# Kernel optimization log

Measured on AMD Instinct MI355X. Metric: run time of the kernel, lower is better.

The kernel has to match this reference:

```python
import jax, jax.numpy as jnp
import numpy as np

N = 100_000   # total nodes per graph batch
E = 400_000   # directed edges per graph batch
G = 1024      # number of graphs
F_IN = 90


def _lin_init(key, fan_in, fan_out):
    s = 1.0 / np.sqrt(fan_in)
    kW, kb = jax.random.split(key)
    W = jax.random.uniform(kW, (fan_in, fan_out), jnp.float32, -s, s)
    b = jax.random.uniform(kb, (fan_out,), jnp.float32, -s, s)
    return W, b


def setup_inputs() -> dict:
    key = jax.random.key(0)
    ks = jax.random.split(key, 16)
    batch = (jnp.arange(N, dtype=jnp.int32) * G // N).astype(jnp.int32)
    inp = {
        'x1': jax.random.normal(ks[0], (N, F_IN), jnp.float32),
        'edge_index1': jax.random.randint(ks[1], (2, E), 0, N, jnp.int32),
        'batch1': batch,
        'x2': jax.random.normal(ks[2], (N, F_IN), jnp.float32),
        'edge_index2': jax.random.randint(ks[3], (2, E), 0, N, jnp.int32),
        'batch2': batch,
    }
    W1, b1 = _lin_init(ks[4], 90, 128)
    W2, b2 = _lin_init(ks[5], 128, 256)
    W3, b3 = _lin_init(ks[6], 256, 256)
    W4, b4 = _lin_init(ks[7], 256, 256)
    fc1_W, fc1_b = _lin_init(ks[8], 1024, 512)
    fc2_W, fc2_b = _lin_init(ks[9], 512, 256)
    fc3_W, fc3_b = _lin_init(ks[10], 256, 1)
    inp.update(W1=W1, b1=b1, W2=W2, b2=b2, W3=W3, b3=b3, W4=W4, b4=b4,
               fc1_W=fc1_W, fc1_b=fc1_b, fc2_W=fc2_W, fc2_b=fc2_b,
               fc3_W=fc3_W, fc3_b=fc3_b)
    return inp


def _gcn(x, W, b, src, dst, dinv):
    # GCNConv: D^{-1/2} (A + I) D^{-1/2} X W + b  (self-loops added)
    h = x @ W                                   # [N, F_out]
    norm = dinv[src] * dinv[dst]                # [E]
    agg = jax.ops.segment_sum(h[src] * norm[:, None], dst, num_segments=N)
    agg = agg + h * (dinv * dinv)[:, None]      # self-loop term
    return agg + b


def _drug_encoder(x, edge_index, batch, W1, b1, W2, b2, W3, b3, W4, b4):
    src, dst = edge_index[0], edge_index[1]
    # degree with self-loops (PyG gcn_norm)
    deg = jax.ops.segment_sum(jnp.ones(src.shape[0], x.dtype), dst, num_segments=N) + 1.0
    dinv = jax.lax.rsqrt(deg)
    x = jax.nn.relu(_gcn(x, W1, b1, src, dst, dinv))
    x = jax.nn.relu(_gcn(x, W2, b2, src, dst, dinv))
    x = jax.nn.relu(_gcn(x, W3, b3, src, dst, dinv))
    x = jax.nn.relu(_gcn(x, W4, b4, src, dst, dinv))
    gmax = jax.ops.segment_max(x, batch, num_segments=G)
    cnt = jax.ops.segment_sum(jnp.ones(N, x.dtype), batch, num_segments=G)
    gmean = jax.ops.segment_sum(x, batch, num_segments=G) / cnt[:, None]
    return jnp.concatenate([gmax, gmean], axis=1)   # [G, 512]


def reference(x1, edge_index1, batch1, x2, edge_index2, batch2,
              W1, b1, W2, b2, W3, b3, W4, b4,
              fc1_W, fc1_b, fc2_W, fc2_b, fc3_W, fc3_b):
    h1 = _drug_encoder(x1, edge_index1, batch1, W1, b1, W2, b2, W3, b3, W4, b4)
    h2 = _drug_encoder(x2, edge_index2, batch2, W1, b1, W2, b2, W3, b3, W4, b4)
    x = jnp.concatenate([h1 - h2, h2 - h1], axis=1)   # [G, 1024]
    x = jax.nn.relu(x @ fc1_W + fc1_b)                # dropout = identity (eval)
    x = jax.nn.relu(x @ fc2_W + fc2_b)
    x = jnp.tanh(x @ fc3_W + fc3_b)
    return x                                          # [G, 1]
```

## Files before the change

kernel.cpp:

```cpp
#include <hip/hip_runtime.h>
#include <hip/hip_bf16.h>

#define NN 100000
#define EE 400000
#define GG 1024

typedef _Float16 half_t;
typedef _Float16 f16x8 __attribute__((ext_vector_type(8)));
typedef float f32x4 __attribute__((ext_vector_type(4)));

#define GLOAD_LDS(g, l) \
    __builtin_amdgcn_global_load_lds((const __attribute__((address_space(1))) void*)(g), \
                                     (__attribute__((address_space(3))) void*)(l), 16, 0, 0)


__global__ void k_count(const int* __restrict__ ei, int* __restrict__ deg) {
    int e = blockIdx.x * blockDim.x + threadIdx.x;
    if (e < EE) atomicAdd(&deg[ei[EE + e]], 1);
}

__global__ void k_scan_bsum(const int* __restrict__ deg, int* __restrict__ bsum) {
    __shared__ int lds[256];
    int t = threadIdx.x;
    int base = blockIdx.x * 1024 + t * 4;
    int s = 0;
#pragma unroll
    for (int i = 0; i < 4; ++i) { int idx = base + i; s += (idx < NN) ? deg[idx] : 0; }
    lds[t] = s;
    __syncthreads();
    for (int off = 128; off > 0; off >>= 1) {
        if (t < off) lds[t] += lds[t + off];
        __syncthreads();
    }
    if (t == 0) bsum[blockIdx.x] = lds[0];
}

__global__ void k_scan_write(const int* __restrict__ deg, const int* __restrict__ bsum,
                             int* __restrict__ rowptr) {
    __shared__ int lds[256];
    __shared__ int blockoff;
    int t = threadIdx.x;
    if (t == 0) {
        int off = 0;
        for (int b = 0; b < (int)blockIdx.x; ++b) off += bsum[b];
        blockoff = off;
    }
    int base = blockIdx.x * 1024 + t * 4;
    int v[4]; int ts = 0;
#pragma unroll
    for (int i = 0; i < 4; ++i) { int idx = base + i; v[i] = (idx < NN) ? deg[idx] : 0; ts += v[i]; }
    lds[t] = ts;
    __syncthreads();
    for (int off = 1; off < 256; off <<= 1) {
        int x = (t >= off) ? lds[t - off] : 0;
        __syncthreads();
        lds[t] += x;
        __syncthreads();
    }
    int excl = lds[t] - ts + blockoff;
#pragma unroll
    for (int i = 0; i < 4; ++i) {
        int idx = base + i;
        if (idx < NN) rowptr[idx] = excl;
        excl += v[i];
    }
    if (blockIdx.x == 0 && t == 0) rowptr[NN] = EE;
}

__global__ void k_dinv(const int* __restrict__ deg, float* __restrict__ dinv) {
    int i = blockIdx.x * blockDim.x + threadIdx.x;
    if (i < NN) dinv[i] = rsqrtf((float)deg[i] + 1.0f);
}

__global__ void k_fill(const int* __restrict__ ei, const int* __restrict__ rowptr,
                       int* __restrict__ cnt, int* __restrict__ col) {
    int e = blockIdx.x * blockDim.x + threadIdx.x;
    if (e < EE) {
        int s = ei[e], d = ei[EE + e];
        int pos = rowptr[d] + atomicAdd(&cnt[d], 1);
        col[pos] = s;
    }
}


template <int F, int R, int KPAD>
__global__ void k_agg_split(const float* __restrict__ x, const float* __restrict__ dinv,
                            const int* __restrict__ rowptr, const int* __restrict__ col,
                            half_t* __restrict__ out) {
    int wave = threadIdx.x >> 6;
    int lane = threadIdx.x & 63;
    int n = blockIdx.x * 4 + wave;
    if (n >= NN) return;
    float dn = dinv[n];
    const float* xr = x + (size_t)n * F;
    float acc[R];
#pragma unroll
    for (int r = 0; r < R; ++r) {
        int f = lane + 64 * r;
        acc[r] = (f < F) ? dn * xr[f] : 0.f;
    }
    int j0 = rowptr[n], j1 = rowptr[n + 1];
    for (int j = j0; j < j1; ++j) {
        int s = col[j];
        float ds = dinv[s];
        const float* xs = x + (size_t)s * F;
#pragma unroll
        for (int r = 0; r < R; ++r) {
            int f = lane + 64 * r;
            if (f < F) acc[r] += ds * xs[f];
        }
    }
    half_t* o = out + (size_t)n * (2 * KPAD);
#pragma unroll
    for (int r = 0; r < R; ++r) {
        int f = lane + 64 * r;
        if (f < F) {
            float v = dn * acc[r];
            half_t h = (half_t)v;
            half_t l = (half_t)(v - (float)h);
            o[f] = h;
            o[KPAD + f] = l;
        } else if (f < KPAD) {
            o[f] = (half_t)0.f;
            o[KPAD + f] = (half_t)0.f;
        }
    }
}


template <int VW>
__global__ void k_agg_splitv(const float* __restrict__ x, const float* __restrict__ dinv,
                             const int* __restrict__ rowptr, const int* __restrict__ col,
                             half_t* __restrict__ out) {
    constexpr int F = 64 * VW;
    typedef float fvec __attribute__((ext_vector_type(VW)));
    int wave = threadIdx.x >> 6;
    int lane = threadIdx.x & 63;
    int n = blockIdx.x * 4 + wave;
    if (n >= NN) return;
    float dn = dinv[n];
    fvec acc = dn * ((const fvec*)(x + (size_t)n * F))[lane];
    int j0 = rowptr[n], j1 = rowptr[n + 1];
    for (int j = j0; j < j1; ++j) {
        int s = col[j];
        float ds = dinv[s];
        acc += ds * ((const fvec*)(x + (size_t)s * F))[lane];
    }
    half_t* o = out + (size_t)n * (2 * F);
    half_t hv[VW], lv[VW];
#pragma unroll
    for (int i = 0; i < VW; ++i) {
        float v = dn * acc[i];
        hv[i] = (half_t)v;
        lv[i] = (half_t)(v - (float)hv[i]);
    }
#pragma unroll
    for (int i = 0; i < VW; ++i) o[lane * VW + i] = hv[i];
#pragma unroll
    for (int i = 0; i < VW; ++i) o[F + lane * VW + i] = lv[i];
}


__global__ void k_wprep(const float* __restrict__ W, half_t* __restrict__ Bt,
                        int K, int Kpad, int Nc) {
    int t = blockIdx.x * 256 + threadIdx.x;
    if (t >= Nc * Kpad) return;
    int n = t / Kpad, kp = t % Kpad;
    half_t h = (half_t)0.f, l = (half_t)0.f;
    if (kp < K) {
        float w = W[(size_t)kp * Nc + n];
        h = (half_t)w;
        l = (half_t)(w - (float)h);
    }
    half_t* o = Bt + (size_t)n * 3 * Kpad;
    o[kp] = h;
    o[Kpad + kp] = h;
    o[2 * Kpad + kp] = l;
}


__global__ void k_split(const float* __restrict__ in, half_t* __restrict__ out, int K) {
    int t = blockIdx.x * 256 + threadIdx.x;
    int row = t / K, k = t % K;
    float v = in[t];
    half_t h = (half_t)v;
    half_t l = (half_t)(v - (float)h);
    half_t* o = out + (size_t)row * 2 * K;
    o[k] = h;
    o[K + k] = l;
}


template <bool RELU>
__global__ __launch_bounds__(256, 2)
void k_mgemm(const half_t* __restrict__ Ap, const half_t* __restrict__ Bt,
             const float* __restrict__ bias, float* __restrict__ C,
             int M, int Kpad, int Nc) {
    __shared__ half_t As[128 * 64];
    __shared__ half_t Bs[128 * 64];
    const int tid = threadIdx.x;
    const int wave = tid >> 6, lane = tid & 63;
    const int wm = wave >> 1, wn = wave & 1;
    const int bm = blockIdx.x * 128, bn = blockIdx.y * 128;
    const int KA = 2 * Kpad, KB = 3 * Kpad;
    const int nkt = KB >> 6;
    const int aTiles = KA >> 6;

    f32x4 acc[4][4] = {};

    const int srow = tid >> 3;
    const int ch = tid & 7;

    for (int kt = 0; kt < nkt; ++kt) {
        int ka0 = ((kt < aTiles) ? kt : (kt - aTiles)) << 6;
        int kb0 = kt << 6;
        __syncthreads();
#pragma unroll
        for (int i = 0; i < 4; ++i) {
            int rl = i * 32 + srow;
            int sch = ch ^ (rl & 7);
            int gr = bm + rl; if (gr >= M) gr = M - 1;
            const half_t* ga = Ap + (size_t)gr * KA + ka0 + sch * 8;
            GLOAD_LDS(ga, (char*)As + i * 4096 + wave * 1024);
        }
#pragma unroll
        for (int i = 0; i < 4; ++i) {
            int rl = i * 32 + srow;
            int sch = ch ^ (rl & 7);
            const half_t* gb = Bt + (size_t)(bn + rl) * KB + kb0 + sch * 8;
            GLOAD_LDS(gb, (char*)Bs + i * 4096 + wave * 1024);
        }
        __syncthreads();
#pragma unroll
        for (int s = 0; s < 2; ++s) {
            f16x8 af[4], bf[4];
#pragma unroll
            for (int i = 0; i < 4; ++i) {
                int row = wm * 64 + i * 16 + (lane & 15);
                int c = s * 4 + (lane >> 4);
                af[i] = *(const f16x8*)&As[row * 64 + ((c ^ (row & 7)) << 3)];
            }
#pragma unroll
            for (int j = 0; j < 4; ++j) {
                int row = wn * 64 + j * 16 + (lane & 15);
                int c = s * 4 + (lane >> 4);
                bf[j] = *(const f16x8*)&Bs[row * 64 + ((c ^ (row & 7)) << 3)];
            }
#pragma unroll
            for (int i = 0; i < 4; ++i)
#pragma unroll
                for (int j = 0; j < 4; ++j)
                    acc[i][j] = __builtin_amdgcn_mfma_f32_16x16x32_f16(af[i], bf[j], acc[i][j], 0, 0, 0);
        }
    }

#pragma unroll
    for (int i = 0; i < 4; ++i) {
#pragma unroll
        for (int j = 0; j < 4; ++j) {
            int cc = bn + wn * 64 + j * 16 + (lane & 15);
            float bv = bias[cc];
            int r0 = bm + wm * 64 + i * 16 + (lane >> 4) * 4;
#pragma unroll
            for (int q = 0; q < 4; ++q) {
                int gr = r0 + q;
                if (gr < M) {
                    float v = acc[i][j][q] + bv;
                    if (RELU) v = fmaxf(v, 0.f);
                    C[(size_t)gr * Nc + cc] = v;
                }
            }
        }
    }
}


__global__ void k_starts(const int* __restrict__ batch, int* __restrict__ gstart) {
    int i = blockIdx.x * blockDim.x + threadIdx.x;
    if (i >= NN) return;
    int b = batch[i];
    if (i == 0) {
        for (int g = 0; g <= b; ++g) gstart[g] = 0;
    } else {
        int pb = batch[i - 1];
        for (int g = pb + 1; g <= b; ++g) gstart[g] = i;
    }
    if (i == NN - 1) {
        for (int g = b + 1; g <= GG; ++g) gstart[g] = NN;
    }
}

__global__ void k_pool(const float* __restrict__ act, const int* __restrict__ gstart,
                       float* __restrict__ h) {
    int g = blockIdx.x;
    int f = threadIdx.x;
    int s = gstart[g], e = gstart[g + 1];
    float mx = 0.f, sm = 0.f;
    for (int i = s; i < e; ++i) {
        float v = act[(size_t)i * 256 + f];
        mx = fmaxf(mx, v);
        sm += v;
    }
    float cnt = (float)(e - s);
    h[(size_t)g * 512 + f] = mx;
    h[(size_t)g * 512 + 256 + f] = (cnt > 0.f) ? sm / cnt : 0.f;
}


__global__ void k_headin_split(const float* __restrict__ h, half_t* __restrict__ xh) {
    int t = blockIdx.x * blockDim.x + threadIdx.x;
    if (t >= GG * 1024) return;
    int g = t >> 10, j = t & 1023;
    const float* h1 = h + (size_t)g * 512;
    const float* h2 = h + (size_t)(GG + g) * 512;
    float v = (j < 512) ? (h1[j] - h2[j]) : (h2[j - 512] - h1[j - 512]);
    half_t hi = (half_t)v;
    half_t lo = (half_t)(v - (float)hi);
    half_t* o = xh + (size_t)g * 2048;
    o[j] = hi;
    o[1024 + j] = lo;
}

__global__ void k_fc3(const float* __restrict__ A, const float* __restrict__ W,
                      const float* __restrict__ b, float* __restrict__ out) {
    int g = blockIdx.x * 4 + (threadIdx.x >> 6);
    int lane = threadIdx.x & 63;
    const float* a = A + (size_t)g * 256;
    float p = a[lane] * W[lane] + a[lane + 64] * W[lane + 64]
            + a[lane + 128] * W[lane + 128] + a[lane + 192] * W[lane + 192];
    for (int off = 32; off > 0; off >>= 1) p += __shfl_down(p, off);
    if (lane == 0) out[g] = tanhf(p + b[0]);
}


extern "C" void kernel_launch(void* const* d_in, const int* in_sizes, int n_in,
                              void* d_out, int out_size, void* d_ws, size_t ws_size,
                              hipStream_t stream) {
    const float* x1  = (const float*)d_in[0];
    const int*   ei1 = (const int*)d_in[1];
    const int*   ba1 = (const int*)d_in[2];
    const float* x2  = (const float*)d_in[3];
    const int*   ei2 = (const int*)d_in[4];
    const int*   ba2 = (const int*)d_in[5];
    const float* W1 = (const float*)d_in[6];
    const float* b1 = (const float*)d_in[7];
    const float* W2 = (const float*)d_in[8];
    const float* b2 = (const float*)d_in[9];
    const float* W3 = (const float*)d_in[10];
    const float* b3 = (const float*)d_in[11];
    const float* W4 = (const float*)d_in[12];
    const float* b4 = (const float*)d_in[13];
    const float* fc1W = (const float*)d_in[14];
    const float* fc1b = (const float*)d_in[15];
    const float* fc2W = (const float*)d_in[16];
    const float* fc2b = (const float*)d_in[17];
    const float* fc3W = (const float*)d_in[18];
    const float* fc3b = (const float*)d_in[19];
    float* out = (float*)d_out;

    char* ws = (char*)d_ws;
    size_t off = 0;
    auto alloc = [&](size_t bytes) -> void* {
        void* p = (void*)(ws + off);
        off += (bytes + 255) & ~(size_t)255;
        return p;
    };
    int*    deg    = (int*)alloc(NN * sizeof(int));
    int*    rowptr = (int*)alloc((NN + 1) * sizeof(int));
    int*    cnt    = (int*)alloc(NN * sizeof(int));
    int*    col    = (int*)alloc(EE * sizeof(int));
    int*    bsum   = (int*)alloc(128 * sizeof(int));
    int*    gstart = (int*)alloc((GG + 1) * sizeof(int));
    float*  dinv   = (float*)alloc(NN * sizeof(float));
    half_t* Ap     = (half_t*)alloc((size_t)NN * 512 * sizeof(half_t));
    float*  act    = (float*)alloc((size_t)NN * 256 * sizeof(float));
    half_t* Bt1    = (half_t*)alloc((size_t)128 * 384 * sizeof(half_t));
    half_t* Bt2    = (half_t*)alloc((size_t)256 * 384 * sizeof(half_t));
    half_t* Bt3    = (half_t*)alloc((size_t)256 * 768 * sizeof(half_t));
    half_t* Bt4    = (half_t*)alloc((size_t)256 * 768 * sizeof(half_t));
    half_t* Btf1   = (half_t*)alloc((size_t)512 * 3072 * sizeof(half_t));
    half_t* Btf2   = (half_t*)alloc((size_t)256 * 1536 * sizeof(half_t));
    float*  hpool  = (float*)alloc((size_t)2 * GG * 512 * sizeof(float));
    half_t* xhs    = (half_t*)alloc((size_t)GG * 2048 * sizeof(half_t));
    float*  t1     = (float*)alloc((size_t)GG * 512 * sizeof(float));
    half_t* t1s    = (half_t*)alloc((size_t)GG * 1024 * sizeof(half_t));
    float*  t2     = (float*)alloc((size_t)GG * 256 * sizeof(float));

    int nsb = (NN + 1023) / 1024;
    int mt = (NN + 127) / 128;

    k_wprep<<<(128 * 128 + 255) / 256, 256, 0, stream>>>(W1, Bt1, 90, 128, 128);
    k_wprep<<<(256 * 128 + 255) / 256, 256, 0, stream>>>(W2, Bt2, 128, 128, 256);
    k_wprep<<<(256 * 256 + 255) / 256, 256, 0, stream>>>(W3, Bt3, 256, 256, 256);
    k_wprep<<<(256 * 256 + 255) / 256, 256, 0, stream>>>(W4, Bt4, 256, 256, 256);
    k_wprep<<<(512 * 1024 + 255) / 256, 256, 0, stream>>>(fc1W, Btf1, 1024, 1024, 512);
    k_wprep<<<(256 * 512 + 255) / 256, 256, 0, stream>>>(fc2W, Btf2, 512, 512, 256);

    for (int p = 0; p < 2; ++p) {
        const float* x   = p ? x2 : x1;
        const int*   ei  = p ? ei2 : ei1;
        const int*   bat = p ? ba2 : ba1;
        hipMemsetAsync(deg, 0, NN * sizeof(int), stream);
        hipMemsetAsync(cnt, 0, NN * sizeof(int), stream);
        k_count<<<(EE + 255) / 256, 256, 0, stream>>>(ei, deg);
        k_scan_bsum<<<nsb, 256, 0, stream>>>(deg, bsum);
        k_scan_write<<<nsb, 256, 0, stream>>>(deg, bsum, rowptr);
        k_dinv<<<(NN + 255) / 256, 256, 0, stream>>>(deg, dinv);
        k_fill<<<(EE + 255) / 256, 256, 0, stream>>>(ei, rowptr, cnt, col);
        k_starts<<<(NN + 255) / 256, 256, 0, stream>>>(bat, gstart);

        k_agg_split<90, 2, 128><<<(NN + 3) / 4, 256, 0, stream>>>(x, dinv, rowptr, col, Ap);
        k_mgemm<true><<<dim3(mt, 1), 256, 0, stream>>>(Ap, Bt1, b1, act, NN, 128, 128);
        k_agg_splitv<2><<<(NN + 3) / 4, 256, 0, stream>>>(act, dinv, rowptr, col, Ap);
        k_mgemm<true><<<dim3(mt, 2), 256, 0, stream>>>(Ap, Bt2, b2, act, NN, 128, 256);
        k_agg_splitv<4><<<(NN + 3) / 4, 256, 0, stream>>>(act, dinv, rowptr, col, Ap);
        k_mgemm<true><<<dim3(mt, 2), 256, 0, stream>>>(Ap, Bt3, b3, act, NN, 256, 256);
        k_agg_splitv<4><<<(NN + 3) / 4, 256, 0, stream>>>(act, dinv, rowptr, col, Ap);
        k_mgemm<true><<<dim3(mt, 2), 256, 0, stream>>>(Ap, Bt4, b4, act, NN, 256, 256);

        k_pool<<<GG, 256, 0, stream>>>(act, gstart, hpool + (size_t)p * GG * 512);
    }

    k_headin_split<<<(GG * 1024 + 255) / 256, 256, 0, stream>>>(hpool, xhs);
    k_mgemm<true><<<dim3(GG / 128, 4), 256, 0, stream>>>(xhs, Btf1, fc1b, t1, GG, 1024, 512);
    k_split<<<(GG * 512 + 255) / 256, 256, 0, stream>>>(t1, t1s, 512);
    k_mgemm<true><<<dim3(GG / 128, 2), 256, 0, stream>>>(t1s, Btf2, fc2b, t2, GG, 512, 256);
    k_fc3<<<GG / 4, 256, 0, stream>>>(t2, fc3W, fc3b, out);
}
```

Before: 1.463 ms.

## Batch CSR build for both graphs, fuse dinv into scan, unroll gather loops

Builds the CSR structure for both encoders in one pass: the degree count, scan, fill and graph-start kernels each run once over concatenated 2N/2E ranges, and dinv is computed inside the scan-write kernel. This removes several launches and memsets. The aggregation kernels unroll the neighbour loop by four so more independent gathers are in flight, and the layer-1 aggregation uses float2 loads over 45 lanes. Column indices for graph 2 stay local to that graph and are paired with an offset rowptr, which is consistent. The single-block serial prefix over bsum now covers twice as many blocks.

```diff
diff --git a/kernel.cpp b/kernel.cpp
--- a/kernel.cpp
+++ b/kernel.cpp
@@ -8,24 +8,30 @@
 typedef _Float16 half_t;
 typedef _Float16 f16x8 __attribute__((ext_vector_type(8)));
 typedef float f32x4 __attribute__((ext_vector_type(4)));
+typedef float f32x2 __attribute__((ext_vector_type(2)));
 
 #define GLOAD_LDS(g, l) \
     __builtin_amdgcn_global_load_lds((const __attribute__((address_space(1))) void*)(g), \
                                      (__attribute__((address_space(3))) void*)(l), 16, 0, 0)
 
 
-__global__ void k_count(const int* __restrict__ ei, int* __restrict__ deg) {
-    int e = blockIdx.x * blockDim.x + threadIdx.x;
-    if (e < EE) atomicAdd(&deg[ei[EE + e]], 1);
-}
-
-__global__ void k_scan_bsum(const int* __restrict__ deg, int* __restrict__ bsum) {
+__global__ void k_count2(const int* __restrict__ ei1, const int* __restrict__ ei2,
+                         int* __restrict__ deg) {
+    int e = blockIdx.x * 256 + threadIdx.x;
+    if (e >= 2 * EE) return;
+    int enc = e >= EE;
+    const int* ei = enc ? ei2 : ei1;
+    int le = e - enc * EE;
+    atomicAdd(&deg[enc * NN + ei[EE + le]], 1);
+}
+
+__global__ void k_scan_bsum(const int* __restrict__ deg, int* __restrict__ bsum, int total) {
     __shared__ int lds[256];
     int t = threadIdx.x;
     int base = blockIdx.x * 1024 + t * 4;
     int s = 0;
 #pragma unroll
-    for (int i = 0; i < 4; ++i) { int idx = base + i; s += (idx < NN) ? deg[idx] : 0; }
+    for (int i = 0; i < 4; ++i) { int idx = base + i; s += (idx < total) ? deg[idx] : 0; }
     lds[t] = s;
     __syncthreads();
     for (int off = 128; off > 0; off >>= 1) {
@@ -36,7 +42,8 @@
 }
 
 __global__ void k_scan_write(const int* __restrict__ deg, const int* __restrict__ bsum,
-                             int* __restrict__ rowptr) {
+                             int* __restrict__ rowptr, float* __restrict__ dinv,
+                             int total, int totedge) {
     __shared__ int lds[256];
     __shared__ int blockoff;
     int t = threadIdx.x;
@@ -48,7 +55,7 @@
     int base = blockIdx.x * 1024 + t * 4;
     int v[4]; int ts = 0;
 #pragma unroll
-    for (int i = 0; i < 4; ++i) { int idx = base + i; v[i] = (idx < NN) ? deg[idx] : 0; ts += v[i]; }
+    for (int i = 0; i < 4; ++i) { int idx = base + i; v[i] = (idx < total) ? deg[idx] : 0; ts += v[i]; }
     lds[t] = ts;
     __syncthreads();
     for (int off = 1; off < 256; off <<= 1) {
@@ -61,72 +68,92 @@
 #pragma unroll
     for (int i = 0; i < 4; ++i) {
         int idx = base + i;
-        if (idx < NN) rowptr[idx] = excl;
+        if (idx < total) {
+            rowptr[idx] = excl;
+            dinv[idx] = rsqrtf((float)v[i] + 1.0f);
+        }
         excl += v[i];
     }
-    if (blockIdx.x == 0 && t == 0) rowptr[NN] = EE;
-}
-
-__global__ void k_dinv(const int* __restrict__ deg, float* __restrict__ dinv) {
-    int i = blockIdx.x * blockDim.x + threadIdx.x;
-    if (i < NN) dinv[i] = rsqrtf((float)deg[i] + 1.0f);
-}
-
-__global__ void k_fill(const int* __restrict__ ei, const int* __restrict__ rowptr,
-                       int* __restrict__ cnt, int* __restrict__ col) {
-    int e = blockIdx.x * blockDim.x + threadIdx.x;
-    if (e < EE) {
-        int s = ei[e], d = ei[EE + e];
-        int pos = rowptr[d] + atomicAdd(&cnt[d], 1);
-        col[pos] = s;
-    }
-}
-
-
-template <int F, int R, int KPAD>
-__global__ void k_agg_split(const float* __restrict__ x, const float* __restrict__ dinv,
-                            const int* __restrict__ rowptr, const int* __restrict__ col,
-                            half_t* __restrict__ out) {
+    if (blockIdx.x == 0 && t == 0) rowptr[total] = totedge;
+}
+
+__global__ void k_fill2(const int* __restrict__ ei1, const int* __restrict__ ei2,
+                        const int* __restrict__ rowptr, int* __restrict__ cnt,
+                        int* __restrict__ colv) {
+    int e = blockIdx.x * 256 + threadIdx.x;
+    if (e >= 2 * EE) return;
+    int enc = e >= EE;
+    const int* ei = enc ? ei2 : ei1;
+    int le = e - enc * EE;
+    int s = ei[le], d = ei[EE + le];
+    int gd = enc * NN + d;
+    int pos = rowptr[gd] + atomicAdd(&cnt[gd], 1);
+    colv[pos] = s;
+}
+
+__global__ void k_starts2(const int* __restrict__ b1, const int* __restrict__ b2,
+                          int* __restrict__ gstart) {
+    int i = blockIdx.x * 256 + threadIdx.x;
+    if (i >= 2 * NN) return;
+    int enc = i >= NN;
+    int il = i - enc * NN;
+    const int* bat = enc ? b2 : b1;
+    int* gs = gstart + enc * (GG + 1);
+    int b = bat[il];
+    if (il == 0) {
+        for (int g = 0; g <= b; ++g) gs[g] = 0;
+    } else {
+        int pb = bat[il - 1];
+        for (int g = pb + 1; g <= b; ++g) gs[g] = il;
+    }
+    if (il == NN - 1) {
+        for (int g = b + 1; g <= GG; ++g) gs[g] = NN;
+    }
+}
+
+
+__global__ void k_agg90(const float* __restrict__ x, const float* __restrict__ dinv,
+                        const int* __restrict__ rowptr, const int* __restrict__ col,
+                        half_t* __restrict__ out) {
     int wave = threadIdx.x >> 6;
     int lane = threadIdx.x & 63;
     int n = blockIdx.x * 4 + wave;
     if (n >= NN) return;
+    bool al = lane < 45;
     float dn = dinv[n];
-    const float* xr = x + (size_t)n * F;
-    float acc[R];
-#pragma unroll
-    for (int r = 0; r < R; ++r) {
-        int f = lane + 64 * r;
-        acc[r] = (f < F) ? dn * xr[f] : 0.f;
-    }
+    f32x2 acc = {0.f, 0.f};
+    if (al) acc = dn * ((const f32x2*)(x + (size_t)n * 90))[lane];
     int j0 = rowptr[n], j1 = rowptr[n + 1];
-    for (int j = j0; j < j1; ++j) {
+    int j = j0;
+    for (; j + 4 <= j1; j += 4) {
+        int s0 = col[j], s1 = col[j + 1], s2 = col[j + 2], s3 = col[j + 3];
+        float d0 = dinv[s0], d1 = dinv[s1], d2 = dinv[s2], d3 = dinv[s3];
+        if (al) {
+            f32x2 v0 = ((const f32x2*)(x + (size_t)s0 * 90))[lane];
+            f32x2 v1 = ((const f32x2*)(x + (size_t)s1 * 90))[lane];
+            f32x2 v2 = ((const f32x2*)(x + (size_t)s2 * 90))[lane];
+            f32x2 v3 = ((const f32x2*)(x + (size_t)s3 * 90))[lane];
+            acc += d0 * v0;
+            acc += d1 * v1;
+            acc += d2 * v2;
+            acc += d3 * v3;
+        }
+    }
+    for (; j < j1; ++j) {
         int s = col[j];
         float ds = dinv[s];
-        const float* xs = x + (size_t)s * F;
-#pragma unroll
-        for (int r = 0; r < R; ++r) {
-            int f = lane + 64 * r;
-            if (f < F) acc[r] += ds * xs[f];
-        }
-    }
-    half_t* o = out + (size_t)n * (2 * KPAD);
-#pragma unroll
-    for (int r = 0; r < R; ++r) {
-        int f = lane + 64 * r;
-        if (f < F) {
-            float v = dn * acc[r];
-            half_t h = (half_t)v;
-            half_t l = (half_t)(v - (float)h);
-            o[f] = h;
-            o[KPAD + f] = l;
-        } else if (f < KPAD) {
-            o[f] = (half_t)0.f;
-            o[KPAD + f] = (half_t)0.f;
-        }
-    }
-}
-
+        if (al) acc += ds * ((const f32x2*)(x + (size_t)s * 90))[lane];
+    }
+    float v0 = al ? dn * acc[0] : 0.f;
+    float v1 = al ? dn * acc[1] : 0.f;
+    half_t h0 = (half_t)v0, l0 = (half_t)(v0 - (float)h0);
+    half_t h1 = (half_t)v1, l1 = (half_t)(v1 - (float)h1);
+    half_t* o = out + (size_t)n * 256;
+    o[2 * lane] = h0;
+    o[2 * lane + 1] = h1;
+    o[128 + 2 * lane] = l0;
+    o[128 + 2 * lane + 1] = l1;
+}
 
 template <int VW>
 __global__ void k_agg_splitv(const float* __restrict__ x, const float* __restrict__ dinv,
@@ -141,10 +168,22 @@
     float dn = dinv[n];
     fvec acc = dn * ((const fvec*)(x + (size_t)n * F))[lane];
     int j0 = rowptr[n], j1 = rowptr[n + 1];
-    for (int j = j0; j < j1; ++j) {
+    int j = j0;
+    for (; j + 4 <= j1; j += 4) {
+        int s0 = col[j], s1 = col[j + 1], s2 = col[j + 2], s3 = col[j + 3];
+        float d0 = dinv[s0], d1 = dinv[s1], d2 = dinv[s2], d3 = dinv[s3];
+        fvec v0 = ((const fvec*)(x + (size_t)s0 * F))[lane];
+        fvec v1 = ((const fvec*)(x + (size_t)s1 * F))[lane];
+        fvec v2 = ((const fvec*)(x + (size_t)s2 * F))[lane];
+        fvec v3 = ((const fvec*)(x + (size_t)s3 * F))[lane];
+        acc += d0 * v0;
+        acc += d1 * v1;
+        acc += d2 * v2;
+        acc += d3 * v3;
+    }
+    for (; j < j1; ++j) {
         int s = col[j];
-        float ds = dinv[s];
-        acc += ds * ((const fvec*)(x + (size_t)s * F))[lane];
+        acc += dinv[s] * ((const fvec*)(x + (size_t)s * F))[lane];
     }
     half_t* o = out + (size_t)n * (2 * F);
     half_t hv[VW], lv[VW];
@@ -274,21 +313,6 @@
     }
 }
 
-
-__global__ void k_starts(const int* __restrict__ batch, int* __restrict__ gstart) {
-    int i = blockIdx.x * blockDim.x + threadIdx.x;
-    if (i >= NN) return;
-    int b = batch[i];
-    if (i == 0) {
-        for (int g = 0; g <= b; ++g) gstart[g] = 0;
-    } else {
-        int pb = batch[i - 1];
-        for (int g = pb + 1; g <= b; ++g) gstart[g] = i;
-    }
-    if (i == NN - 1) {
-        for (int g = b + 1; g <= GG; ++g) gstart[g] = NN;
-    }
-}
 
 __global__ void k_pool(const float* __restrict__ act, const int* __restrict__ gstart,
                        float* __restrict__ h) {
@@ -365,13 +389,12 @@
         off += (bytes + 255) & ~(size_t)255;
         return p;
     };
-    int*    deg    = (int*)alloc(NN * sizeof(int));
-    int*    rowptr = (int*)alloc((NN + 1) * sizeof(int));
-    int*    cnt    = (int*)alloc(NN * sizeof(int));
-    int*    col    = (int*)alloc(EE * sizeof(int));
-    int*    bsum   = (int*)alloc(128 * sizeof(int));
-    int*    gstart = (int*)alloc((GG + 1) * sizeof(int));
-    float*  dinv   = (float*)alloc(NN * sizeof(float));
+    int*    dc     = (int*)alloc((size_t)4 * NN * sizeof(int));
+    int*    rowptr = (int*)alloc((size_t)(2 * NN + 1) * sizeof(int));
+    int*    colv   = (int*)alloc((size_t)2 * EE * sizeof(int));
+    int*    bsum   = (int*)alloc(256 * sizeof(int));
+    int*    gstart = (int*)alloc((size_t)2 * (GG + 1) * sizeof(int));
+    float*  dinv   = (float*)alloc((size_t)2 * NN * sizeof(float));
     half_t* Ap     = (half_t*)alloc((size_t)NN * 512 * sizeof(half_t));
     float*  act    = (float*)alloc((size_t)NN * 256 * sizeof(float));
     half_t* Bt1    = (half_t*)alloc((size_t)128 * 384 * sizeof(half_t));
@@ -386,7 +409,10 @@
     half_t* t1s    = (half_t*)alloc((size_t)GG * 1024 * sizeof(half_t));
     float*  t2     = (float*)alloc((size_t)GG * 256 * sizeof(float));
 
-    int nsb = (NN + 1023) / 1024;
+    int* deg = dc;
+    int* cnt = dc + 2 * NN;
+
+    int nsb2 = (2 * NN + 1023) / 1024;
     int mt = (NN + 127) / 128;
 
     k_wprep<<<(128 * 128 + 255) / 256, 256, 0, stream>>>(W1, Bt1, 90, 128, 128);
@@ -396,29 +422,29 @@
     k_wprep<<<(512 * 1024 + 255) / 256, 256, 0, stream>>>(fc1W, Btf1, 1024, 1024, 512);
     k_wprep<<<(256 * 512 + 255) / 256, 256, 0, stream>>>(fc2W, Btf2, 512, 512, 256);
 
+    hipMemsetAsync(dc, 0, (size_t)4 * NN * sizeof(int), stream);
+    k_count2<<<(2 * EE + 255) / 256, 256, 0, stream>>>(ei1, ei2, deg);
+    k_scan_bsum<<<nsb2, 256, 0, stream>>>(deg, bsum, 2 * NN);
+    k_scan_write<<<nsb2, 256, 0, stream>>>(deg, bsum, rowptr, dinv, 2 * NN, 2 * EE);
+    k_fill2<<<(2 * EE + 255) / 256, 256, 0, stream>>>(ei1, ei2, rowptr, cnt, colv);
+    k_starts2<<<(2 * NN + 255) / 256, 256, 0, stream>>>(ba1, ba2, gstart);
+
     for (int p = 0; p < 2; ++p) {
-        const float* x   = p ? x2 : x1;
-        const int*   ei  = p ? ei2 : ei1;
-        const int*   bat = p ? ba2 : ba1;
-        hipMemsetAsync(deg, 0, NN * sizeof(int), stream);
-        hipMemsetAsync(cnt, 0, NN * sizeof(int), stream);
-        k_count<<<(EE + 255) / 256, 256, 0, stream>>>(ei, deg);
-        k_scan_bsum<<<nsb, 256, 0, stream>>>(deg, bsum);
-        k_scan_write<<<nsb, 256, 0, stream>>>(deg, bsum, rowptr);
-        k_dinv<<<(NN + 255) / 256, 256, 0, stream>>>(deg, dinv);
-        k_fill<<<(EE + 255) / 256, 256, 0, stream>>>(ei, rowptr, cnt, col);
-        k_starts<<<(NN + 255) / 256, 256, 0, stream>>>(bat, gstart);
-
-        k_agg_split<90, 2, 128><<<(NN + 3) / 4, 256, 0, stream>>>(x, dinv, rowptr, col, Ap);
+        const float* x    = p ? x2 : x1;
+        const int*   rp   = rowptr + p * NN;
+        const float* dv   = dinv + p * NN;
+        const int*   gs   = gstart + p * (GG + 1);
+
+        k_agg90<<<(NN + 3) / 4, 256, 0, stream>>>(x, dv, rp, colv, Ap);
         k_mgemm<true><<<dim3(mt, 1), 256, 0, stream>>>(Ap, Bt1, b1, act, NN, 128, 128);
-        k_agg_splitv<2><<<(NN + 3) / 4, 256, 0, stream>>>(act, dinv, rowptr, col, Ap);
+        k_agg_splitv<2><<<(NN + 3) / 4, 256, 0, stream>>>(act, dv, rp, colv, Ap);
         k_mgemm<true><<<dim3(mt, 2), 256, 0, stream>>>(Ap, Bt2, b2, act, NN, 128, 256);
-        k_agg_splitv<4><<<(NN + 3) / 4, 256, 0, stream>>>(act, dinv, rowptr, col, Ap);
+        k_agg_splitv<4><<<(NN + 3) / 4, 256, 0, stream>>>(act, dv, rp, colv, Ap);
         k_mgemm<true><<<dim3(mt, 2), 256, 0, stream>>>(Ap, Bt3, b3, act, NN, 256, 256);
-        k_agg_splitv<4><<<(NN + 3) / 4, 256, 0, stream>>>(act, dinv, rowptr, col, Ap);
+        k_agg_splitv<4><<<(NN + 3) / 4, 256, 0, stream>>>(act, dv, rp, colv, Ap);
         k_mgemm<true><<<dim3(mt, 2), 256, 0, stream>>>(Ap, Bt4, b4, act, NN, 256, 256);
 
-        k_pool<<<GG, 256, 0, stream>>>(act, gstart, hpool + (size_t)p * GG * 512);
+        k_pool<<<GG, 256, 0, stream>>>(act, gs, hpool + (size_t)p * GG * 512);
     }
 
     k_headin_split<<<(GG * 1024 + 255) / 256, 256, 0, stream>>>(hpool, xhs);
```

Result: faster. 1.351 ms (-7.6%).
